# Kernel optimization log

Measured on AMD Instinct MI355X. Metric: run time of the kernel, lower is better.

## Reference

```python
import jax, jax.numpy as jnp
import numpy as np

LAMBDA_FGW = 0.5
TAU_KL = 0.1
N_OUTER = 5
N_SINKHORN = 10
DIM = 512


def _pdist(a, b):
    # sqrt(clamp(||a-b||^2, 1e-6)) computed via expansion (avoids BxKxMxD temp)
    n2 = ((a * a).sum(-1)[:, :, None] + (b * b).sum(-1)[:, None, :]
          - 2.0 * jnp.einsum('bkd,bmd->bkm', a, b))
    return jnp.sqrt(jnp.clip(n2, 1e-6, None))


def setup_inputs() -> dict:
    key = jax.random.key(0)
    ks = jax.random.split(key, 10)
    B, K, M, D = 256, 128, 128, DIM
    inp = {
        'sq': jax.random.normal(ks[0], (B, K, D), jnp.float32),
        'sr': jax.random.normal(ks[1], (B, M, D), jnp.float32),
        'mask_q': jax.random.uniform(ks[2], (B, K), jnp.float32),
        'mask_r': jax.random.uniform(ks[3], (B, M), jnp.float32),
        'centroids_q': jax.random.normal(ks[4], (B, K, D), jnp.float32),
        'centroids_r': jax.random.normal(ks[5], (B, M, D), jnp.float32),
        'W1': jax.random.normal(ks[6], (D, D), jnp.float32) * 0.02,
        'b1': jnp.zeros((D,), jnp.float32),
        'W2': jax.random.normal(ks[7], (D, D), jnp.float32) * 0.02,
        'b2': jnp.zeros((D,), jnp.float32),
        'log_eps': jnp.asarray(np.log(0.05), jnp.float32),
    }
    return inp


def reference(sq, sr, mask_q, mask_r, centroids_q, centroids_r, W1, b1, W2, b2, log_eps):
    proj = lambda x: jax.nn.relu(x @ W1 + b1) @ W2 + b2
    pq, pr = proj(sq), proj(sr)
    C = _pdist(pq, pr)                      # [B,K,M]
    Sq = _pdist(centroids_q, centroids_q)   # [B,K,K]
    Sr = _pdist(centroids_r, centroids_r)   # [B,M,M]

    mu = mask_q / (mask_q.sum(-1, keepdims=True) + 1e-8)  # [B,K]
    nu = mask_r / (mask_r.sum(-1, keepdims=True) + 1e-8)  # [B,M]
    T = mu[:, :, None] * nu[:, None, :]

    eps = jnp.clip(jnp.exp(log_eps), 0.01, 0.5)
    rho = TAU_KL / (TAU_KL + eps)
    log_mu = jnp.log(jnp.clip(mu, 1e-8, None))
    log_nu = jnp.log(jnp.clip(nu, 1e-8, None))
    Sq2, Sr2 = Sq * Sq, Sr * Sr

    C_fgw = C
    for _ in range(N_OUTER):
        t1 = jnp.einsum('bkl,bl->bk', Sq2, T.sum(2))[:, :, None]
        t2 = jnp.einsum('bm,bmn->bn', T.sum(1), Sr2)[:, None, :]
        L_gw = t1 + t2 - 2.0 * jnp.einsum('bkl,blm->bkm', Sq, jnp.einsum('blm,bmn->bln', T, Sr))
        C_fgw = (1.0 - LAMBDA_FGW) * C + LAMBDA_FGW * L_gw
        log_K = -C_fgw / eps
        log_u = jnp.zeros_like(mu)
        log_v = jnp.zeros_like(nu)
        for _ in range(N_SINKHORN):
            log_u = rho * (log_mu - jax.nn.logsumexp(log_K + log_v[:, None, :], axis=2))
            log_v = rho * (log_nu - jax.nn.logsumexp(log_K + log_u[:, :, None], axis=1))
        T = jnp.exp(log_u[:, :, None] + log_K + log_v[:, None, :])

    cost = (T * C_fgw).sum((-1, -2))
    similarity = jax.nn.sigmoid(-cost)
    return similarity, T, C, cost
```

## Files before the change

kernel.cpp:

```cpp
#include <hip/hip_runtime.h>
#include <math.h>

typedef unsigned short u16;
typedef __attribute__((ext_vector_type(4))) float f32x4;
typedef __attribute__((ext_vector_type(8))) short bf16x8;
typedef __attribute__((ext_vector_type(4))) unsigned short u16x4;
typedef __attribute__((ext_vector_type(8))) unsigned short u16x8;

#define DEVI static __device__ __forceinline__

DEVI float b2f(u16 u){ union{float f; unsigned i;} v; v.i = ((unsigned)u)<<16; return v.f; }
DEVI u16 f2b(float f){ union{float f; unsigned i;} v; v.f=f;
  unsigned r = v.i + 0x7fffu + ((v.i>>16)&1u); return (u16)(r>>16); }
DEVI float u2f(unsigned u){ union{unsigned i; float f;} v; v.i=u; return v.f; }

DEVI unsigned cvtpk(float a, float b){
  unsigned r;
  asm("v_cvt_pk_bf16_f32 %0, %1, %2" : "=v"(r) : "v"(a), "v"(b));
  return r;
}

DEVI void split4(const f32x4 x, u16x4* hi4, u16x4* lo4){
  unsigned h0 = cvtpk(x[0], x[1]);
  unsigned h1 = cvtpk(x[2], x[3]);
  unsigned l0 = cvtpk(x[0]-u2f(h0<<16), x[1]-u2f(h0&0xffff0000u));
  unsigned l1 = cvtpk(x[2]-u2f(h1<<16), x[3]-u2f(h1&0xffff0000u));
  union{unsigned u[2]; u16x4 v;} H,L;
  H.u[0]=h0; H.u[1]=h1; L.u[0]=l0; L.u[1]=l1;
  *hi4 = H.v; *lo4 = L.v;
}

DEVI void gload_lds16(const void* g, void* l){
  __builtin_amdgcn_global_load_lds((const __attribute__((address_space(1))) void*)g,
                                   (__attribute__((address_space(3))) void*)l, 16, 0, 0);
}

DEVI void lds_bar(){ asm volatile("s_waitcnt lgkmcnt(0)\n\ts_barrier" ::: "memory"); }

DEVI f32x4 vmax4(f32x4 a, f32x4 b){
  f32x4 r; r[0]=fmaxf(a[0],b[0]); r[1]=fmaxf(a[1],b[1]);
  r[2]=fmaxf(a[2],b[2]); r[3]=fmaxf(a[3],b[3]); return r;
}

__global__ void prologue_k(const float* __restrict__ W1, const float* __restrict__ W2,
                           u16* __restrict__ W1T, u16* __restrict__ W2T,
                           const float* __restrict__ mask_q, const float* __restrict__ mask_r,
                           float* __restrict__ lmu2, float* __restrict__ lnu2,
                           float* __restrict__ mu, float* __restrict__ nu){
  const int blk = blockIdx.x;
  if (blk < 2048){
    const float* W = (blk<1024)? W1 : W2;
    u16* Wt = (blk<1024)? W1T : W2T;
    int id = (blk&1023)*256 + threadIdx.x;
    int k = id>>9, c = id&511;
    Wt[c*512 + k] = f2b(W[id]);
  } else {
    __shared__ float red[2][4];
    const int h = threadIdx.x>>7, t = threadIdx.x&127;
    const int b = (blk-2048)*2 + h;
    float mq = mask_q[b*128+t], mr = mask_r[b*128+t];
    float s1 = mq, s2 = mr;
    #pragma unroll
    for (int off=1;off<64;off<<=1){ s1 += __shfl_xor(s1,off); s2 += __shfl_xor(s2,off); }
    if ((t&63)==0){ red[h][(t>>6)&1] = s1; red[h][2+((t>>6)&1)] = s2; }
    __syncthreads();
    float sumq = red[h][0]+red[h][1], sumr = red[h][2]+red[h][3];
    float muv = mq/(sumq+1e-8f), nuv = mr/(sumr+1e-8f);
    lmu2[b*128+t] = __log2f(fmaxf(muv,1e-8f));
    lnu2[b*128+t] = __log2f(fmaxf(nuv,1e-8f));
    mu[b*128+t] = muv;
    nu[b*128+t] = nuv;
  }
}

template<int ACT, int NORM, int AF32>
__global__ __launch_bounds__(256) void gemm_k(const u16* __restrict__ X,
    const float* __restrict__ Xf1, const float* __restrict__ Xf2,
    const u16* __restrict__ Wt, const float* __restrict__ bias, u16* __restrict__ OUT,
    float* __restrict__ NP4){
  __shared__ __align__(16) u16 smem[17920];
  u16* sA = smem;
  u16* sB = smem + 8192;
  const int tid = threadIdx.x, wave = tid>>6, lane = tid&63;
  const int bid = (blockIdx.x&7)*256 + (blockIdx.x>>3);
  const int rblk = bid>>2, cb = (bid&3)<<7;
  const u16* Xb = AF32 ? nullptr : (X + (size_t)rblk*(128*512));
  const float* Xbf = AF32 ? (rblk<256 ? Xf1 + (size_t)rblk*65536
                                      : Xf2 + (size_t)(rblk-256)*65536) : nullptr;
  const u16* Wb = Wt + (size_t)cb*512;
  const int lrow = lane&15, lg = lane>>4, wr = wave>>1, wc = wave&1;
  f32x4 acc[4][4] = {};
  for (int s=0;s<8;s++){
    const int k0 = s<<6;
    #pragma unroll
    for (int q=0;q<4;q++){
      const int i = (wave<<2)+q;
      const int row = (i<<3) + (lane>>3);
      const int cd = (lane&7) ^ (row&7);
      if (AF32){
        const float* src = Xbf + row*512 + k0 + (cd<<3);
        const f32x4 va = *(const f32x4*)src;
        const f32x4 vb = *(const f32x4*)(src+4);
        union{unsigned u[4]; u16x8 v;} U;
        U.u[0]=cvtpk(va[0],va[1]); U.u[1]=cvtpk(va[2],va[3]);
        U.u[2]=cvtpk(vb[0],vb[1]); U.u[3]=cvtpk(vb[2],vb[3]);
        *(u16x8*)((char*)sA + i*1024 + lane*16) = U.v;
      } else {
        gload_lds16(Xb + row*512 + k0 + (cd<<3), sA + i*512);
      }
      gload_lds16(Wb + row*512 + k0 + (cd<<3), sB + i*512);
    }
    __syncthreads();
    #pragma unroll
    for (int kh=0;kh<2;kh++){
      bf16x8 a_[4], b_[4];
      #pragma unroll
      for (int i=0;i<4;i++){
        const int ra = (wr<<6)+(i<<4)+lrow;
        a_[i] = *(const bf16x8*)(sA + ra*64 + ((((kh<<2)+lg)^(ra&7))<<3));
        const int rb = (wc<<6)+(i<<4)+lrow;
        b_[i] = *(const bf16x8*)(sB + rb*64 + ((((kh<<2)+lg)^(rb&7))<<3));
      }
      #pragma unroll
      for (int i=0;i<4;i++)
        #pragma unroll
        for (int j=0;j<4;j++)
          acc[i][j] = __builtin_amdgcn_mfma_f32_16x16x32_bf16(a_[i], b_[j], acc[i][j], 0,0,0);
    }
    __syncthreads();
  }
  #pragma unroll
  for (int j=0;j<4;j++){
    const int colb = (wc<<6) + (j<<4) + lrow;
    const float bv = bias[cb + colb];
    #pragma unroll
    for (int i=0;i<4;i++){
      const int rowb = (wr<<6)+(i<<4)+(lg<<2);
      float v0 = acc[i][j][0]+bv, v1 = acc[i][j][1]+bv;
      float v2 = acc[i][j][2]+bv, v3 = acc[i][j][3]+bv;
      if (ACT){ v0=fmaxf(v0,0.f); v1=fmaxf(v1,0.f); v2=fmaxf(v2,0.f); v3=fmaxf(v3,0.f); }
      unsigned pA = cvtpk(v0,v1), pB = cvtpk(v2,v3);
      smem[(rowb  )*140 + colb] = (u16)pA;
      smem[(rowb+1)*140 + colb] = (u16)(pA>>16);
      smem[(rowb+2)*140 + colb] = (u16)pB;
      smem[(rowb+3)*140 + colb] = (u16)(pB>>16);
    }
  }
  __syncthreads();
  const int chunk = lane&15, rql = lane>>4;
  float ns[8];
  #pragma unroll
  for (int it=0; it<8; it++){
    const int rowb = it*16 + wave*4 + rql;
    u16x8 v8 = *(const u16x8*)(smem + rowb*140 + chunk*8);
    *(u16x8*)(OUT + (size_t)((rblk<<7)+rowb)*512 + cb + chunk*8) = v8;
    if (NORM){
      float s = 0.f;
      #pragma unroll
      for (int e=0;e<8;e++){ float f = b2f(v8[e]); s = fmaf(f,f,s); }
      s += __shfl_xor(s,1); s += __shfl_xor(s,2);
      s += __shfl_xor(s,4); s += __shfl_xor(s,8);
      ns[it] = s;
    }
  }
  if (NORM && chunk==0){
    #pragma unroll
    for (int it=0;it<8;it++)
      NP4[(size_t)(bid&3)*65536 + (rblk<<7) + it*16 + wave*4 + rql] = ns[it];
  }
}

__global__ __launch_bounds__(256) void pdist_all_k(const u16* __restrict__ PQ,
    const float* __restrict__ NP4, const float* __restrict__ cq,
    const float* __restrict__ cr, float* __restrict__ Cm,
    char* __restrict__ SQHL, char* __restrict__ SRHL){
  __shared__ __align__(16) u16 sA[8192];
  __shared__ __align__(16) u16 sB[8192];
  __shared__ float nA[128], nB[128];
  const int tid = threadIdx.x, wave = tid>>6, lane = tid&63;
  const int lrow = lane&15, lg = lane>>4, wr = wave>>1, wc = wave&1;
  const int b = blockIdx.x & 255;

  if (blockIdx.x < 256){
    if (tid < 128){
      const int row = b*128 + tid;
      nA[tid] = NP4[row] + NP4[65536+row] + NP4[131072+row] + NP4[196608+row];
    } else {
      const int row = 32768 + b*128 + (tid-128);
      nB[tid-128] = NP4[row] + NP4[65536+row] + NP4[131072+row] + NP4[196608+row];
    }
    const u16* Ab = PQ + (size_t)b*(128*512);
    const u16* Bb = PQ + (size_t)(32768 + b*128)*512;
    f32x4 acc[4][4] = {};
    for (int s=0;s<8;s++){
      const int k0 = s<<6;
      #pragma unroll
      for (int q=0;q<4;q++){
        const int i = (wave<<2)+q;
        const int row = (i<<3) + (lane>>3);
        const int cd = (lane&7) ^ (row&7);
        gload_lds16(Ab + row*512 + k0 + (cd<<3), sA + i*512);
        gload_lds16(Bb + row*512 + k0 + (cd<<3), sB + i*512);
      }
      __syncthreads();
      #pragma unroll
      for (int kh=0;kh<2;kh++){
        bf16x8 a_[4], b_[4];
        #pragma unroll
        for (int i=0;i<4;i++){
          const int ra = (wr<<6)+(i<<4)+lrow;
          a_[i] = *(const bf16x8*)(sA + ra*64 + ((((kh<<2)+lg)^(ra&7))<<3));
          const int rb = (wc<<6)+(i<<4)+lrow;
          b_[i] = *(const bf16x8*)(sB + rb*64 + ((((kh<<2)+lg)^(rb&7))<<3));
        }
        #pragma unroll
        for (int i=0;i<4;i++)
          #pragma unroll
          for (int j=0;j<4;j++)
            acc[i][j] = __builtin_amdgcn_mfma_f32_16x16x32_bf16(a_[i], b_[j], acc[i][j], 0,0,0);
      }
      __syncthreads();
    }
    #pragma unroll
    for (int j=0;j<4;j++){
      const int col = (wc<<6)+(j<<4)+lrow;
      const float nbv = nB[col];
      #pragma unroll
      for (int i=0;i<4;i++){
        const int row0 = (wr<<6)+(i<<4)+(lg<<2);
        #pragma unroll
        for (int r=0;r<4;r++){
          float n2 = nA[row0+r] + nbv - 2.0f*acc[i][j][r];
          Cm[(size_t)b*16384 + (size_t)(row0+r)*128 + col] = sqrtf(fmaxf(n2, 1e-6f));
        }
      }
    }
  } else {
    const float* Sb = ((blockIdx.x < 512)? cq : cr) + (size_t)b*65536;
    char* SHL = (blockIdx.x < 512)? SQHL : SRHL;
    f32x4 acc[4][4] = {};
    float nacc[4] = {0.f,0.f,0.f,0.f};
    for (int s=0;s<8;s++){
      const int k0 = s<<6;
      #pragma unroll
      for (int q=0;q<4;q++){
        const int i = (wave<<2)+q;
        const int row = (i<<3) + (lane>>3);
        const int cd = (lane&7) ^ (row&7);
        const float* src = Sb + row*512 + k0 + (cd<<3);
        const f32x4 va = *(const f32x4*)src;
        const f32x4 vb = *(const f32x4*)(src+4);
        union{unsigned u[4]; u16x8 v;} U;
        U.u[0]=cvtpk(va[0],va[1]); U.u[1]=cvtpk(va[2],va[3]);
        U.u[2]=cvtpk(vb[0],vb[1]); U.u[3]=cvtpk(vb[2],vb[3]);
        #pragma unroll
        for (int p2=0;p2<4;p2++){
          float f0 = u2f(U.u[p2]<<16), f1 = u2f(U.u[p2]&0xffff0000u);
          nacc[q] = fmaf(f0,f0,nacc[q]);
          nacc[q] = fmaf(f1,f1,nacc[q]);
        }
        *(u16x8*)((char*)sA + i*1024 + lane*16) = U.v;
      }
      __syncthreads();
      #pragma unroll
      for (int kh=0;kh<2;kh++){
        bf16x8 a_[4], b_[4];
        #pragma unroll
        for (int i=0;i<4;i++){
          const int ra = (wr<<6)+(i<<4)+lrow;
          a_[i] = *(const bf16x8*)(sA + ra*64 + ((((kh<<2)+lg)^(ra&7))<<3));
          const int rb = (wc<<6)+(i<<4)+lrow;
          b_[i] = *(const bf16x8*)(sA + rb*64 + ((((kh<<2)+lg)^(rb&7))<<3));
        }
        #pragma unroll
        for (int i=0;i<4;i++)
          #pragma unroll
          for (int j=0;j<4;j++)
            acc[i][j] = __builtin_amdgcn_mfma_f32_16x16x32_bf16(a_[i], b_[j], acc[i][j], 0,0,0);
      }
      __syncthreads();
    }
    #pragma unroll
    for (int q=0;q<4;q++){
      float v = nacc[q];
      v += __shfl_xor(v,1); v += __shfl_xor(v,2); v += __shfl_xor(v,4);
      if ((lane&7)==0) nA[((wave<<2)+q)*8 + (lane>>3)] = v;
    }
    __syncthreads();
    #pragma unroll
    for (int j=0;j<4;j++){
      const int col = (wc<<6)+(j<<4)+lrow;
      const float nbv = nA[col];
      #pragma unroll
      for (int i=0;i<4;i++){
        const int row0 = (wr<<6)+(i<<4)+(lg<<2);
        f32x4 sv;
        #pragma unroll
        for (int r=0;r<4;r++){
          float n2 = nA[row0+r] + nbv - 2.0f*acc[i][j][r];
          sv[r] = sqrtf(fmaxf(n2, 1e-6f));
        }
        u16x4 hi4, lo4;
        split4(sv, &hi4, &lo4);
        const int sa = col*256 + ((((row0>>3)^col)&15)<<4) + ((row0&7)<<1);
        char* base = SHL + (size_t)b*65536;
        *(u16x4*)(base + sa) = hi4;
        *(u16x4*)(base + 32768 + sa) = lo4;
      }
    }
  }
}

__global__ __launch_bounds__(512,1) void fgw_loop_k(
    const char* __restrict__ SQHL, const char* __restrict__ SRHL,
    const float* __restrict__ C_g,
    const float* __restrict__ MU, const float* __restrict__ NU,
    const float* __restrict__ LMU2, const float* __restrict__ LNU2,
    const float* __restrict__ log_eps,
    float* __restrict__ T_out, float* __restrict__ cost_out, float* __restrict__ sim_out)
{
  __shared__ __align__(16) char bufT[65536];
  __shared__ __align__(16) char bufS[65536];
  __shared__ __align__(16) float avs[128], bvs[128], t1s[128], t2s[128];
  __shared__ __align__(16) float lus[128], lvs[128];
  __shared__ float redc[8];

  const int b = blockIdx.x, tid = threadIdx.x;
  const int w = tid>>6, lane = tid&63, l15 = lane&15, lg = lane>>4;
  const char* SqHLb = SQHL + (size_t)b*65536;
  const char* SrHLb = SRHL + (size_t)b*65536;
  const float* Cb   = C_g + (size_t)b*16384;
  const float* MUb  = MU + b*128;
  const float* NUb  = NU + b*128;

  float eps = __expf(log_eps[0]); eps = fminf(fmaxf(eps,0.01f),0.5f);
  const float rho = 0.1f/(0.1f+eps);
  const float hscale = 0.5f*1.4426950408889634f/eps;

  const int kR = 16*w + l15;
  const int n0 = 16*w + 4*lg;
  const float lmu2R = LMU2[b*128+kR];
  const float lnu2C = LNU2[b*128+kR];

  const int rowA256 = (16*w + l15)*256;
  const int glo2 = lg ^ (l15 & 3);
  const int ghi2 = l15 & 12;
  const int wtail = l15*256 + ((((2*w + (lg>>1)) ^ l15)&15)<<4) + ((lg&1)<<3);
  const int slotW = lg*16 + (l15^lg);

  f32x4 Cf2[8];
  #pragma unroll
  for (int kt=0;kt<8;kt++)
    Cf2[kt] = -hscale * (*(const f32x4*)(Cb + (size_t)(16*kt+l15)*128 + n0));

  f32x4 lkR[8], lkC[8];
  float luR = 0.f, lvC = 0.f;

  #pragma unroll
  for (int r2=0;r2<8;r2++)
    gload_lds16(SrHLb + r2*8192 + tid*16, bufS + r2*8192 + tid*16);

  for (int outer=0; outer<5; outer++){
    {
      f32x4 avp = {0.f,0.f,0.f,0.f};
      #pragma unroll
      for (int q=0;q<8;q++){
        f32x4 TR;
        if (outer==0){
          const f32x4 nu4 = *(const f32x4*)(NUb + 16*q + 4*lg);
          TR = MUb[kR]*nu4;
        } else {
          const f32x4 lv4 = *(const f32x4*)&lvs[16*q + 4*lg];
          #pragma unroll
          for (int e=0;e<4;e++) TR[e] = exp2f(lkR[q][e] + luR + lv4[e]);
        }
        u16x4 hi4, lo4;
        split4(TR, &hi4, &lo4);
        const int sa = kR*256 + ((((2*q+(lg>>1)) ^ l15)&15)<<4) + ((lg&1)<<3);
        *(u16x4*)(bufT + sa) = hi4;
        *(u16x4*)(bufT + 32768 + sa) = lo4;
        avp += TR;
      }
      float av = avp[0]+avp[1]+avp[2]+avp[3];
      av += __shfl_xor(av,16); av += __shfl_xor(av,32);
      if (lg==0){
        avs[kR] = av;
        bvs[kR] = (outer==0) ? NUb[kR] : exp2f(lnu2C - 10.f*eps*lvC);
      }
    }
    __syncthreads();

    f32x4 sqr[8];
    #pragma unroll
    for (int r2=0;r2<8;r2++)
      sqr[r2] = *(const f32x4*)(SqHLb + r2*8192 + tid*16);
    {
      const int p = tid>>2, sub = tid&3;
      float s2 = 0.f;
      #pragma unroll
      for (int gg=0; gg<4; gg++){
        const int g = 4*sub+gg;
        const int off = p*256 + (((g ^ (p&15))&15)<<4);
        const u16x8 h8 = *(const u16x8*)(bufS + off);
        const u16x8 l8 = *(const u16x8*)(bufS + 32768 + off);
        const f32x4 bva = *(const f32x4*)&bvs[8*g];
        const f32x4 bvb = *(const f32x4*)&bvs[8*g+4];
        #pragma unroll
        for (int e=0;e<4;e++){
          float x = b2f(h8[e]) + b2f(l8[e]);
          s2 = fmaf(bva[e], x*x, s2);
          float y2 = b2f(h8[4+e]) + b2f(l8[4+e]);
          s2 = fmaf(bvb[e], y2*y2, s2);
        }
      }
      s2 += __shfl_xor(s2,1); s2 += __shfl_xor(s2,2);
      if (sub==0) t2s[p] = s2;
    }
    f32x4 acc1[8] = {};
    #pragma unroll
    for (int qt=0;qt<4;qt++){
      const int colOff = (((4*qt) ^ ghi2) | glo2) << 4;
      const bf16x8 ahi = *(const bf16x8*)(bufT + rowA256 + colOff);
      const bf16x8 alo = *(const bf16x8*)(bufT + 32768 + rowA256 + colOff);
      const int bbase = l15*256 + colOff;
      #pragma unroll
      for (int nt=0;nt<8;nt++){
        const bf16x8 bhi = *(const bf16x8*)(bufS + nt*4096 + bbase);
        const bf16x8 blo = *(const bf16x8*)(bufS + 32768 + nt*4096 + bbase);
        acc1[nt] = __builtin_amdgcn_mfma_f32_16x16x32_bf16(ahi, bhi, acc1[nt], 0,0,0);
        acc1[nt] = __builtin_amdgcn_mfma_f32_16x16x32_bf16(ahi, blo, acc1[nt], 0,0,0);
        acc1[nt] = __builtin_amdgcn_mfma_f32_16x16x32_bf16(alo, bhi, acc1[nt], 0,0,0);
      }
    }
    __syncthreads();

    #pragma unroll
    for (int r2=0;r2<8;r2++)
      *(f32x4*)(bufS + r2*8192 + tid*16) = sqr[r2];
    #pragma unroll
    for (int nt=0;nt<8;nt++){
      u16x4 hi4, lo4;
      split4(acc1[nt], &hi4, &lo4);
      const int sa = nt*4096 + wtail;
      *(u16x4*)(bufT + sa) = hi4;
      *(u16x4*)(bufT + 32768 + sa) = lo4;
    }
    __syncthreads();

    {
      const int p = tid>>2, sub = tid&3;
      float s1 = 0.f;
      #pragma unroll
      for (int gg=0; gg<4; gg++){
        const int g = 4*sub+gg;
        const int off = p*256 + (((g ^ (p&15))&15)<<4);
        const u16x8 h8 = *(const u16x8*)(bufS + off);
        const u16x8 l8 = *(const u16x8*)(bufS + 32768 + off);
        const f32x4 ava = *(const f32x4*)&avs[8*g];
        const f32x4 avb = *(const f32x4*)&avs[8*g+4];
        #pragma unroll
        for (int e=0;e<4;e++){
          float x = b2f(h8[e]) + b2f(l8[e]);
          s1 = fmaf(ava[e], x*x, s1);
          float y2 = b2f(h8[4+e]) + b2f(l8[4+e]);
          s1 = fmaf(avb[e], y2*y2, s1);
        }
      }
      s1 += __shfl_xor(s1,1); s1 += __shfl_xor(s1,2);
      if (sub==0) t1s[p] = s1;
    }
    f32x4 acc2[8] = {};
    #pragma unroll
    for (int qt=0;qt<4;qt++){
      const int colOff = (((4*qt) ^ ghi2) | glo2) << 4;
      const bf16x8 ahi = *(const bf16x8*)(bufT + rowA256 + colOff);
      const bf16x8 alo = *(const bf16x8*)(bufT + 32768 + rowA256 + colOff);
      const int bbase = l15*256 + colOff;
      #pragma unroll
      for (int kt=0;kt<8;kt++){
        const bf16x8 bhi = *(const bf16x8*)(bufS + kt*4096 + bbase);
        const bf16x8 blo = *(const bf16x8*)(bufS + 32768 + kt*4096 + bbase);
        acc2[kt] = __builtin_amdgcn_mfma_f32_16x16x32_bf16(ahi, bhi, acc2[kt], 0,0,0);
        acc2[kt] = __builtin_amdgcn_mfma_f32_16x16x32_bf16(ahi, blo, acc2[kt], 0,0,0);
        acc2[kt] = __builtin_amdgcn_mfma_f32_16x16x32_bf16(alo, bhi, acc2[kt], 0,0,0);
      }
    }
    __syncthreads();

    if (outer<4){
      #pragma unroll
      for (int r2=0;r2<8;r2++)
        gload_lds16(SrHLb + r2*8192 + tid*16, bufS + r2*8192 + tid*16);
    }
    f32x4 lkf[8];
    {
      const f32x4 t24 = *(const f32x4*)&t2s[n0];
      #pragma unroll
      for (int kt=0;kt<8;kt++){
        const float t1v = t1s[16*kt+l15];
        lkf[kt] = Cf2[kt] + hscale*(2.0f*acc2[kt] - t1v - t24);
      }
    }
    #pragma unroll
    for (int kt=0;kt<8;kt++)
      *(f32x4*)(bufT + (((kt*8+w)*64 + slotW)<<4)) = lkf[kt];
    lds_bar();
    #pragma unroll
    for (int q=0;q<8;q++)
      lkR[q] = *(const f32x4*)(bufT + (((w*8+q)*64 + slotW)<<4));
    #pragma unroll
    for (int q=0;q<8;q++){
      #pragma unroll
      for (int e=0;e<4;e++){
        const int slotC = (l15>>2)*16 + ((4*lg+e) ^ (l15>>2));
        lkC[q][e] = *(const float*)(bufT + (((q*8+w)*64 + slotC)<<4) + ((l15&3)<<2));
      }
    }

    for (int it=0; it<10; it++){
      f32x4 y[8];
      #pragma unroll
      for (int q=0;q<8;q++){
        y[q] = lkR[q];
        if (it) y[q] += *(const f32x4*)&lvs[16*q+4*lg];
      }
      f32x4 m4 = vmax4(vmax4(vmax4(y[0],y[1]),vmax4(y[2],y[3])),
                       vmax4(vmax4(y[4],y[5]),vmax4(y[6],y[7])));
      float mx = fmaxf(fmaxf(m4[0],m4[1]), fmaxf(m4[2],m4[3]));
      mx = fmaxf(mx,__shfl_xor(mx,16)); mx = fmaxf(mx,__shfl_xor(mx,32));
      f32x4 s4 = {0.f,0.f,0.f,0.f};
      #pragma unroll
      for (int q=0;q<8;q++){
        #pragma unroll
        for (int e=0;e<4;e++) s4[e] += exp2f(y[q][e]-mx);
      }
      float s = s4[0]+s4[1]+s4[2]+s4[3];
      s += __shfl_xor(s,16); s += __shfl_xor(s,32);
      luR = rho*(lmu2R - (mx + __log2f(s)));
      if (lg==0) lus[kR] = luR;
      lds_bar();
      #pragma unroll
      for (int q=0;q<8;q++)
        y[q] = lkC[q] + *(const f32x4*)&lus[16*q+4*lg];
      m4 = vmax4(vmax4(vmax4(y[0],y[1]),vmax4(y[2],y[3])),
                 vmax4(vmax4(y[4],y[5]),vmax4(y[6],y[7])));
      mx = fmaxf(fmaxf(m4[0],m4[1]), fmaxf(m4[2],m4[3]));
      mx = fmaxf(mx,__shfl_xor(mx,16)); mx = fmaxf(mx,__shfl_xor(mx,32));
      s4 = (f32x4){0.f,0.f,0.f,0.f};
      #pragma unroll
      for (int q=0;q<8;q++){
        #pragma unroll
        for (int e=0;e<4;e++) s4[e] += exp2f(y[q][e]-mx);
      }
      s = s4[0]+s4[1]+s4[2]+s4[3];
      s += __shfl_xor(s,16); s += __shfl_xor(s,32);
      lvC = rho*(lnu2C - (mx + __log2f(s)));
      if (lg==0) lvs[kR] = lvC;
      lds_bar();
    }

    if (outer==4){
      float cp = 0.f;
      float* Tb = T_out + (size_t)b*16384;
      #pragma unroll
      for (int q=0;q<8;q++){
        const f32x4 lv4 = *(const f32x4*)&lvs[16*q+4*lg];
        f32x4 t;
        #pragma unroll
        for (int e=0;e<4;e++) t[e] = exp2f(lkR[q][e] + luR + lv4[e]);
        *(f32x4*)(Tb + kR*128 + 16*q + 4*lg) = t;
        const f32x4 pr = t*lkR[q];
        cp += pr[0]+pr[1]+pr[2]+pr[3];
      }
      cp *= -eps*0.6931471805599453f;
      #pragma unroll
      for (int off=1;off<64;off<<=1) cp += __shfl_xor(cp, off);
      if (lane==0) redc[w] = cp;
      __syncthreads();
      if (tid==0){
        float tot = 0.f;
        #pragma unroll
        for (int w2=0;w2<8;w2++) tot += redc[w2];
        cost_out[b] = tot;
        sim_out[b]  = 1.0f/(1.0f + __expf(tot));
      }
    }
  }
}

extern "C" void kernel_launch(void* const* d_in, const int* in_sizes, int n_in,
                              void* d_out, int out_size, void* d_ws, size_t ws_size,
                              hipStream_t stream){
  const float* sq      = (const float*)d_in[0];
  const float* sr      = (const float*)d_in[1];
  const float* mask_q  = (const float*)d_in[2];
  const float* mask_r  = (const float*)d_in[3];
  const float* cq      = (const float*)d_in[4];
  const float* cr      = (const float*)d_in[5];
  const float* W1      = (const float*)d_in[6];
  const float* b1      = (const float*)d_in[7];
  const float* W2      = (const float*)d_in[8];
  const float* b2      = (const float*)d_in[9];
  const float* log_eps = (const float*)d_in[10];

  float* out  = (float*)d_out;
  float* sim  = out;
  float* Tm   = out + 256;
  float* Cm   = Tm + 4194304;
  float* cost = Cm + 4194304;

  char* ws = (char*)d_ws;
  size_t off = 0;
  auto alloc = [&](size_t bytes)->void*{ void* p = ws + off; off += (bytes+255)&~(size_t)255; return p; };
  u16*   PQ  = (u16*)  alloc(67108864);
  u16*   HQ  = (u16*)  alloc(67108864);
  u16*   W1T = (u16*)  alloc(524288);
  u16*   W2T = (u16*)  alloc(524288);
  float* NP4 = (float*)alloc(1048576);
  float* LMU = (float*)alloc(131072);
  float* LNU = (float*)alloc(131072);
  float* MUA = (float*)alloc(131072);
  float* NUA = (float*)alloc(131072);
  (void)ws_size; (void)in_sizes; (void)n_in; (void)out_size;

  char* SQHL = (char*)PQ;
  char* SRHL = (char*)PQ + 16777216;

  prologue_k<<<2176,256,0,stream>>>(W1, W2, W1T, W2T, mask_q, mask_r,
                                    LMU, LNU, MUA, NUA);
  gemm_k<1,0,1><<<2048,256,0,stream>>>(nullptr, sq, sr, W1T, b1, HQ, nullptr);
  gemm_k<0,1,0><<<2048,256,0,stream>>>(HQ, nullptr, nullptr, W2T, b2, PQ, NP4);
  pdist_all_k<<<768,256,0,stream>>>(PQ, NP4, cq, cr, Cm, SQHL, SRHL);
  fgw_loop_k<<<256,512,0,stream>>>(SQHL, SRHL, Cm, MUA, NUA, LMU, LNU,
                                   log_eps, Tm, cost, sim);
}
```

Baseline: 399.2 us.

## Enlarge projection GEMM tiles to 256x128 with 512-thread blocks

The projection GEMMs now use 512-thread blocks that each compute a 256-row by 128-column output tile instead of 128x128. The grid is halved, and each weight tile loaded into shared memory is reused across twice as many rows, which cuts redundant weight traffic and block count. The epilogue is staged in two halves through the shared buffer with extra barriers. The larger shared footprint and block size may lower occupancy.

New measurement: 391.1 us. 1.02x faster.

```diff
diff --git a/kernel.cpp b/kernel.cpp
--- a/kernel.cpp
+++ b/kernel.cpp
@@ -74,29 +74,36 @@
 }
 
 template<int ACT, int NORM, int AF32>
-__global__ __launch_bounds__(256) void gemm_k(const u16* __restrict__ X,
+__global__ __launch_bounds__(512) void gemm_k(const u16* __restrict__ X,
     const float* __restrict__ Xf1, const float* __restrict__ Xf2,
     const u16* __restrict__ Wt, const float* __restrict__ bias, u16* __restrict__ OUT,
     float* __restrict__ NP4){
-  __shared__ __align__(16) u16 smem[17920];
+  __shared__ __align__(16) u16 smem[24576];
   u16* sA = smem;
-  u16* sB = smem + 8192;
+  u16* sB = smem + 16384;
   const int tid = threadIdx.x, wave = tid>>6, lane = tid&63;
-  const int bid = (blockIdx.x&7)*256 + (blockIdx.x>>3);
+  const int bid = (blockIdx.x&7)*128 + (blockIdx.x>>3);
   const int rblk = bid>>2, cb = (bid&3)<<7;
-  const u16* Xb = AF32 ? nullptr : (X + (size_t)rblk*(128*512));
-  const float* Xbf = AF32 ? (rblk<256 ? Xf1 + (size_t)rblk*65536
-                                      : Xf2 + (size_t)(rblk-256)*65536) : nullptr;
+  const u16* Xb = AF32 ? nullptr : (X + (size_t)rblk*131072);
+  const float* Xbf = AF32 ? (rblk<128 ? Xf1 + (size_t)rblk*131072
+                                      : Xf2 + (size_t)(rblk-128)*131072) : nullptr;
   const u16* Wb = Wt + (size_t)cb*512;
   const int lrow = lane&15, lg = lane>>4, wr = wave>>1, wc = wave&1;
   f32x4 acc[4][4] = {};
   for (int s=0;s<8;s++){
     const int k0 = s<<6;
     #pragma unroll
+    for (int q=0;q<2;q++){
+      const int g = (wave*2+q)*64 + lane;
+      const int row = g>>3;
+      const int cd = (g&7) ^ (row&7);
+      gload_lds16(Wb + row*512 + k0 + (cd<<3), (char*)sB + (wave*2+q)*1024 + lane*16);
+    }
+    #pragma unroll
     for (int q=0;q<4;q++){
-      const int i = (wave<<2)+q;
-      const int row = (i<<3) + (lane>>3);
-      const int cd = (lane&7) ^ (row&7);
+      const int g = (wave*4+q)*64 + lane;
+      const int row = g>>3;
+      const int cd = (g&7) ^ (row&7);
       if (AF32){
         const float* src = Xbf + row*512 + k0 + (cd<<3);
         const f32x4 va = *(const f32x4*)src;
@@ -104,11 +111,10 @@
         union{unsigned u[4]; u16x8 v;} U;
         U.u[0]=cvtpk(va[0],va[1]); U.u[1]=cvtpk(va[2],va[3]);
         U.u[2]=cvtpk(vb[0],vb[1]); U.u[3]=cvtpk(vb[2],vb[3]);
-        *(u16x8*)((char*)sA + i*1024 + lane*16) = U.v;
+        *(u16x8*)((char*)sA + (wave*4+q)*1024 + lane*16) = U.v;
       } else {
-        gload_lds16(Xb + row*512 + k0 + (cd<<3), sA + i*512);
-      }
-      gload_lds16(Wb + row*512 + k0 + (cd<<3), sB + i*512);
+        gload_lds16(Xb + row*512 + k0 + (cd<<3), (char*)sA + (wave*4+q)*1024 + lane*16);
+      }
     }
     __syncthreads();
     #pragma unroll
@@ -130,43 +136,44 @@
     __syncthreads();
   }
   #pragma unroll
-  for (int j=0;j<4;j++){
-    const int colb = (wc<<6) + (j<<4) + lrow;
-    const float bv = bias[cb + colb];
-    #pragma unroll
-    for (int i=0;i<4;i++){
-      const int rowb = (wr<<6)+(i<<4)+(lg<<2);
-      float v0 = acc[i][j][0]+bv, v1 = acc[i][j][1]+bv;
-      float v2 = acc[i][j][2]+bv, v3 = acc[i][j][3]+bv;
-      if (ACT){ v0=fmaxf(v0,0.f); v1=fmaxf(v1,0.f); v2=fmaxf(v2,0.f); v3=fmaxf(v3,0.f); }
-      unsigned pA = cvtpk(v0,v1), pB = cvtpk(v2,v3);
-      smem[(rowb  )*140 + colb] = (u16)pA;
-      smem[(rowb+1)*140 + colb] = (u16)(pA>>16);
-      smem[(rowb+2)*140 + colb] = (u16)pB;
-      smem[(rowb+3)*140 + colb] = (u16)(pB>>16);
-    }
-  }
-  __syncthreads();
-  const int chunk = lane&15, rql = lane>>4;
-  float ns[8];
-  #pragma unroll
-  for (int it=0; it<8; it++){
-    const int rowb = it*16 + wave*4 + rql;
-    u16x8 v8 = *(const u16x8*)(smem + rowb*140 + chunk*8);
-    *(u16x8*)(OUT + (size_t)((rblk<<7)+rowb)*512 + cb + chunk*8) = v8;
-    if (NORM){
-      float s = 0.f;
-      #pragma unroll
-      for (int e=0;e<8;e++){ float f = b2f(v8[e]); s = fmaf(f,f,s); }
-      s += __shfl_xor(s,1); s += __shfl_xor(s,2);
-      s += __shfl_xor(s,4); s += __shfl_xor(s,8);
-      ns[it] = s;
-    }
-  }
-  if (NORM && chunk==0){
-    #pragma unroll
-    for (int it=0;it<8;it++)
-      NP4[(size_t)(bid&3)*65536 + (rblk<<7) + it*16 + wave*4 + rql] = ns[it];
+  for (int h=0; h<2; h++){
+    if ((wave>>2) == h){
+      #pragma unroll
+      for (int j=0;j<4;j++){
+        const int colb = (wc<<6) + (j<<4) + lrow;
+        const float bv = bias[cb + colb];
+        #pragma unroll
+        for (int i=0;i<4;i++){
+          const int lr = ((wr&1)<<6)+(i<<4)+(lg<<2);
+          float v0 = acc[i][j][0]+bv, v1 = acc[i][j][1]+bv;
+          float v2 = acc[i][j][2]+bv, v3 = acc[i][j][3]+bv;
+          if (ACT){ v0=fmaxf(v0,0.f); v1=fmaxf(v1,0.f); v2=fmaxf(v2,0.f); v3=fmaxf(v3,0.f); }
+          unsigned pA = cvtpk(v0,v1), pB = cvtpk(v2,v3);
+          smem[(lr  )*140 + colb] = (u16)pA;
+          smem[(lr+1)*140 + colb] = (u16)(pA>>16);
+          smem[(lr+2)*140 + colb] = (u16)pB;
+          smem[(lr+3)*140 + colb] = (u16)(pB>>16);
+        }
+      }
+    }
+    __syncthreads();
+    const int chunk = tid&15, rsub = tid>>4;
+    #pragma unroll
+    for (int it=0; it<4; it++){
+      const int lr = it*32 + rsub;
+      u16x8 v8 = *(const u16x8*)(smem + lr*140 + chunk*8);
+      *(u16x8*)(OUT + (size_t)(rblk*256 + h*128 + lr)*512 + cb + chunk*8) = v8;
+      if (NORM){
+        float sn = 0.f;
+        #pragma unroll
+        for (int e=0;e<8;e++){ float f = b2f(v8[e]); sn = fmaf(f,f,sn); }
+        sn += __shfl_xor(sn,1); sn += __shfl_xor(sn,2);
+        sn += __shfl_xor(sn,4); sn += __shfl_xor(sn,8);
+        if (chunk==0)
+          NP4[(size_t)(bid&3)*65536 + rblk*256 + h*128 + lr] = sn;
+      }
+    }
+    __syncthreads();
   }
 }
 
@@ -628,8 +635,8 @@
 
   prologue_k<<<2176,256,0,stream>>>(W1, W2, W1T, W2T, mask_q, mask_r,
                                     LMU, LNU, MUA, NUA);
-  gemm_k<1,0,1><<<2048,256,0,stream>>>(nullptr, sq, sr, W1T, b1, HQ, nullptr);
-  gemm_k<0,1,0><<<2048,256,0,stream>>>(HQ, nullptr, nullptr, W2T, b2, PQ, NP4);
+  gemm_k<1,0,1><<<1024,512,0,stream>>>(nullptr, sq, sr, W1T, b1, HQ, nullptr);
+  gemm_k<0,1,0><<<1024,512,0,stream>>>(HQ, nullptr, nullptr, W2T, b2, PQ, NP4);
   pdist_all_k<<<768,256,0,stream>>>(PQ, NP4, cq, cr, Cm, SQHL, SRHL);
   fgw_loop_k<<<256,512,0,stream>>>(SQHL, SRHL, Cm, MUA, NUA, LMU, LNU,
                                    log_eps, Tm, cost, sim);
```
